# Kernel tuning notes

Measured on AMD Instinct MI355X. Metric: run time of the kernel, lower is better.

The kernel has to match this reference:

```python
import jax, jax.numpy as jnp
import numpy as np


def setup_inputs() -> dict:
    key = jax.random.key(0)
    k1, k2, k3 = jax.random.split(key, 3)
    B, T, C = 4, 2048, 1024
    dim = C
    x = jax.random.normal(k1, (B, T, C), dtype=jnp.float32)
    # torch nn.Linear weight layout: [out_features, in_features], scaled like kaiming-uniform-ish
    w_qkv = jax.random.normal(k2, (3 * dim, dim), dtype=jnp.float32) * (1.0 / np.sqrt(dim))
    w_out = jax.random.normal(k3, (dim, dim), dtype=jnp.float32) * (1.0 / np.sqrt(dim))
    return {"x": x, "w_qkv": w_qkv, "w_out": w_out}


def reference(x, w_qkv, w_out):
    B, T, C = x.shape
    n_heads = 16
    head_dim = C // n_heads

    qkv = jnp.einsum("btc,dc->btd", x, w_qkv)  # [B,T,3C]
    q, k, v = jnp.split(qkv, 3, axis=-1)

    def split_heads(t):
        return t.reshape(B, T, n_heads, head_dim).transpose(0, 2, 1, 3)  # [B,H,T,hd]

    q, k, v = split_heads(q), split_heads(k), split_heads(v)

    scale = 1.0 / np.sqrt(head_dim).astype(np.float32)
    scores = jnp.einsum("bhqd,bhkd->bhqk", q, k) * scale  # [B,H,T,T]
    causal = jnp.tril(jnp.ones((T, T), dtype=bool))
    scores = jnp.where(causal, scores, jnp.finfo(scores.dtype).min)
    attn = jax.nn.softmax(scores, axis=-1)
    out = jnp.einsum("bhqk,bhkd->bhqd", attn, v)  # [B,H,T,hd]
    out = out.transpose(0, 2, 1, 3).reshape(B, T, C)
    return jnp.einsum("btc,dc->btd", out, w_out)
```

## Files before the change

kernel.cpp:

```cpp
#include <hip/hip_runtime.h>
#include <hip/hip_bf16.h>


typedef __attribute__((ext_vector_type(8))) short bf16x8;
typedef __attribute__((ext_vector_type(4))) float f32x4;
typedef __attribute__((ext_vector_type(16))) float f32x16;
typedef __attribute__((ext_vector_type(2))) unsigned uint2v;

#define GLOBAL_AS __attribute__((address_space(1)))
#define LDS_AS __attribute__((address_space(3)))

__device__ __forceinline__ unsigned short f2b_rne(float f) {
  unsigned u = __float_as_uint(f);
  unsigned r = u + 0x7fffu + ((u >> 16) & 1u);
  return (unsigned short)(r >> 16);
}

__device__ __forceinline__ unsigned cvt_pk_bf16(float lo, float hi) {
  unsigned r;
  asm("v_cvt_pk_bf16_f32 %0, %1, %2" : "=v"(r) : "v"(lo), "v"(hi));
  return r;
}

__device__ __forceinline__ void gload_lds16(const void* g, void* l) {
  __builtin_amdgcn_global_load_lds((const GLOBAL_AS void*)g, (LDS_AS void*)l, 16, 0, 0);
}

__global__ void f32_to_bf16_vec(const float* __restrict__ src,
                                unsigned short* __restrict__ dst, int n4) {
  int i = blockIdx.x * blockDim.x + threadIdx.x;
  int stride = gridDim.x * blockDim.x;
  for (; i < n4; i += stride) {
    float4 v = reinterpret_cast<const float4*>(src)[i];
    ushort4 o;
    o.x = f2b_rne(v.x); o.y = f2b_rne(v.y);
    o.z = f2b_rne(v.z); o.w = f2b_rne(v.w);
    reinterpret_cast<ushort4*>(dst)[i] = o;
  }
}

__global__ __launch_bounds__(256)
void v_transpose(const unsigned short* __restrict__ qkv,
                 unsigned short* __restrict__ vt) {
  __shared__ __align__(16) unsigned short Ts[64][64];
  const int tc = blockIdx.x, bh = blockIdx.y;
  const int b = bh >> 4, hed = bh & 15;
  const int t0 = tc * 64;
  const int tid = threadIdx.x;
  {
    const int r = tid >> 2, cb = (tid & 3) * 2;
    const unsigned short* src =
        qkv + (size_t)(b * 2048 + t0 + r) * 3072 + 2048 + hed * 64;
    bf16x8 v0 = *(const bf16x8*)(src + cb * 8);
    bf16x8 v1 = *(const bf16x8*)(src + cb * 8 + 8);
    *(bf16x8*)&Ts[r][(cb ^ (r & 7)) * 8] = v0;
    *(bf16x8*)&Ts[r][((cb + 1) ^ (r & 7)) * 8] = v1;
  }
  __syncthreads();
  const int d = tid >> 2;
  unsigned short* dst = vt + ((size_t)bh * 64 + d) * 2048 + t0;
#pragma unroll
  for (int tb2 = 0; tb2 < 2; ++tb2) {
    int tb = (tid & 3) * 2 + tb2;
    union { unsigned short s[8]; bf16x8 v; } o;
#pragma unroll
    for (int i = 0; i < 8; ++i) {
      int row = tb * 8 + i;
      o.s[i] = Ts[row][(((d >> 3) ^ (row & 7)) * 8) + (d & 7)];
    }
    *(bf16x8*)(dst + tb * 8) = o.v;
  }
}

__global__ __launch_bounds__(512, 2)
void gemm_qkv(const unsigned short* __restrict__ A,
              const unsigned short* __restrict__ B,
              unsigned short* __restrict__ C) {
  const int K = 1024, N = 3072;
  __shared__ __align__(16) unsigned short As[2][2][128 * 64];
  __shared__ __align__(16) unsigned short Bs[2][128 * 64];

  const int tid = threadIdx.x, wid = tid >> 6, lane = tid & 63;
  const int l31 = lane & 31, h = lane >> 5;
  const int wgid = ((int)blockIdx.x & 7) * 96 + ((int)blockIdx.x >> 3);
  const int bx = wgid % 24, by = wgid / 24;
  const int m0 = by * 256, n0 = bx * 128;
  const int wr = wid >> 1, wc = wid & 1;

  auto stage = [&](int t, int buf) {
    const int k0 = t * 64;
    const int r8 = lane >> 3;
    const int blk = (lane & 7) ^ r8;
#pragma unroll
    for (int hh = 0; hh < 2; ++hh)
#pragma unroll
      for (int r = 0; r < 2; ++r) {
        int row = r * 64 + wid * 8 + r8;
        gload_lds16(A + (size_t)(m0 + hh * 128 + row) * K + k0 + blk * 8,
                    &As[buf][hh][r * 4096 + wid * 512]);
      }
#pragma unroll
    for (int r = 0; r < 2; ++r) {
      int row = r * 64 + wid * 8 + r8;
      gload_lds16(B + (size_t)(n0 + row) * K + k0 + blk * 8,
                  &Bs[buf][r * 4096 + wid * 512]);
    }
  };

  f32x16 acc[2][2] = {};

  stage(0, 0);
  asm volatile("s_waitcnt vmcnt(0)" ::: "memory");
  __builtin_amdgcn_sched_barrier(0);
  __builtin_amdgcn_s_barrier();
  __builtin_amdgcn_sched_barrier(0);

  int cur = 0;
  for (int t = 0; t < 16; ++t) {
    if (t + 1 < 16) stage(t + 1, cur ^ 1);

    bf16x8 af[2][4], bfr[2][4];
#pragma unroll
    for (int mi = 0; mi < 2; ++mi) {
      int row = (wr & 1) * 64 + mi * 32 + l31;
#pragma unroll
      for (int ks = 0; ks < 4; ++ks) {
        int chunk = (ks * 2 + h) ^ (row & 7);
        af[mi][ks] = *(const bf16x8*)&As[cur][wr >> 1][row * 64 + chunk * 8];
      }
    }
#pragma unroll
    for (int ni = 0; ni < 2; ++ni) {
      int row = wc * 64 + ni * 32 + l31;
#pragma unroll
      for (int ks = 0; ks < 4; ++ks) {
        int chunk = (ks * 2 + h) ^ (row & 7);
        bfr[ni][ks] = *(const bf16x8*)&Bs[cur][row * 64 + chunk * 8];
      }
    }
    __builtin_amdgcn_s_setprio(1);
#pragma unroll
    for (int ks = 0; ks < 4; ++ks)
#pragma unroll
      for (int mi = 0; mi < 2; ++mi)
#pragma unroll
        for (int ni = 0; ni < 2; ++ni)
          acc[mi][ni] = __builtin_amdgcn_mfma_f32_32x32x16_bf16(
              af[mi][ks], bfr[ni][ks], acc[mi][ni], 0, 0, 0);
    __builtin_amdgcn_s_setprio(0);

    asm volatile("s_waitcnt vmcnt(0)" ::: "memory");
    __builtin_amdgcn_sched_barrier(0);
    __builtin_amdgcn_s_barrier();
    __builtin_amdgcn_sched_barrier(0);
    cur ^= 1;
  }

#pragma unroll
  for (int mi = 0; mi < 2; ++mi)
#pragma unroll
    for (int ni = 0; ni < 2; ++ni)
#pragma unroll
      for (int reg = 0; reg < 16; ++reg) {
        int row = m0 + wr * 64 + mi * 32 + (reg & 3) + 8 * (reg >> 2) + 4 * h;
        int col = n0 + wc * 64 + ni * 32 + l31;
        C[(size_t)row * N + col] = f2b_rne(acc[mi][ni][reg]);
      }
}

__global__ __launch_bounds__(256)
void gemm_nt(const unsigned short* __restrict__ A,
             const unsigned short* __restrict__ B,
             float* __restrict__ Cout, int M, int N, int K) {
  __shared__ __align__(16) unsigned short As[128][32];
  __shared__ __align__(16) unsigned short Bs[128][32];
  const int tid = threadIdx.x;
  const int w = tid >> 6, lane = tid & 63;
  const int l16 = lane & 15, lg = lane >> 4;
  const int wrow = (w >> 1) * 64, wcol = (w & 1) * 64;
  const int m0 = blockIdx.y * 128, n0 = blockIdx.x * 128;

  f32x4 acc[4][4] = {};

  auto stage = [&](int k0) {
#pragma unroll
    for (int c2 = 0; c2 < 2; ++c2) {
      int c = 2 * w + c2;
      const unsigned short* ga =
          A + (size_t)(m0 + 16 * c + (lane >> 2)) * K + k0 + (lane & 3) * 8;
      gload_lds16(ga, &As[16 * c][0]);
      const unsigned short* gb =
          B + (size_t)(n0 + 16 * c + (lane >> 2)) * K + k0 + (lane & 3) * 8;
      gload_lds16(gb, &Bs[16 * c][0]);
    }
  };

  stage(0);
  __syncthreads();
  const int nk = K >> 5;
  for (int ks = 0; ks < nk; ++ks) {
    bf16x8 af[4], bfr[4];
#pragma unroll
    for (int mi = 0; mi < 4; ++mi)
      af[mi] = *(const bf16x8*)&As[wrow + mi * 16 + l16][lg * 8];
#pragma unroll
    for (int ni = 0; ni < 4; ++ni)
      bfr[ni] = *(const bf16x8*)&Bs[wcol + ni * 16 + l16][lg * 8];
    __syncthreads();
    if (ks + 1 < nk) stage((ks + 1) * 32);
#pragma unroll
    for (int mi = 0; mi < 4; ++mi)
#pragma unroll
      for (int ni = 0; ni < 4; ++ni)
        acc[mi][ni] = __builtin_amdgcn_mfma_f32_16x16x32_bf16(
            af[mi], bfr[ni], acc[mi][ni], 0, 0, 0);
    __syncthreads();
  }

#pragma unroll
  for (int mi = 0; mi < 4; ++mi)
#pragma unroll
    for (int ni = 0; ni < 4; ++ni)
#pragma unroll
      for (int j = 0; j < 4; ++j) {
        int row = m0 + wrow + mi * 16 + lg * 4 + j;
        int col = n0 + wcol + ni * 16 + l16;
        Cout[(size_t)row * N + col] = acc[mi][ni][j];
      }
}

__global__ __launch_bounds__(256)
void attn_fwd(const unsigned short* __restrict__ qkv,
              const unsigned short* __restrict__ vt,
              unsigned short* __restrict__ out) {
  const int T = 2048, C3 = 3072;
  __shared__ __align__(16) unsigned short Ks[2][64][64];
  __shared__ __align__(16) unsigned short Vs[2][64][64];
  __shared__ float Bc[4][32];

  const int tid = threadIdx.x, w = tid >> 6, lane = tid & 63;
  const int l31 = lane & 31, h = lane >> 5;
  const int wgid = (blockIdx.x & 7) * 128 + (blockIdx.x >> 3);
  const int qt = 15 - (wgid & 15);
  const int bh = wgid >> 4;
  const int b = bh >> 4, hed = bh & 15;
  const int qw = qt * 128 + w * 32;
  const size_t rowbase = (size_t)b * T * C3;
  const int hoff = hed * 64;
  const unsigned short* vbase = vt + (size_t)bh * 64 * 2048;
  const float c2 = 0.18033688f;

  auto stageK = [&](int kv0, int buf) {
#pragma unroll
    for (int pp = 0; pp < 2; ++pp) {
      int chunk = w * 2 + pp;
      int row = chunk * 8 + (lane >> 3);
      int blk = (lane & 7) ^ (lane >> 3);
      gload_lds16(
          qkv + rowbase + (size_t)(kv0 + row) * C3 + 1024 + hoff + blk * 8,
          &Ks[buf][chunk * 8][0]);
    }
  };
  auto stageV = [&](int kv0, int buf) {
#pragma unroll
    for (int pp = 0; pp < 2; ++pp) {
      int chunk = w * 2 + pp;
      int drow = chunk * 8 + (lane >> 3);
      int blk = (lane & 7) ^ (lane >> 3);
      gload_lds16(vbase + (size_t)drow * 2048 + kv0 + blk * 8,
                  &Vs[buf][chunk * 8][0]);
    }
  };

  bf16x8 qf[4];
  {
    const unsigned short* qp =
        qkv + rowbase + (size_t)(qw + l31) * C3 + hoff + h * 8;
#pragma unroll
    for (int s = 0; s < 4; ++s) qf[s] = *(const bf16x8*)(qp + 16 * s);
  }

  f32x16 oacc[2] = {};
  float m_r = -1e30f, sum = 0.f;

  stageK(0, 0);
  stageV(0, 0);

  int cur = 0;
  const int ntiles = qt * 2 + 2;
  for (int t = 0; t < ntiles; ++t) {
    const int kv0 = t * 64;
    __builtin_amdgcn_s_barrier();
    if (t + 1 < ntiles) {
      stageK(kv0 + 64, cur ^ 1);
      stageV(kv0 + 64, cur ^ 1);
      asm volatile("s_waitcnt vmcnt(4)" ::: "memory");
    } else {
      asm volatile("s_waitcnt vmcnt(0)" ::: "memory");
    }
    __builtin_amdgcn_s_barrier();
    __builtin_amdgcn_sched_barrier(0);

    if (kv0 <= qw) {
      f32x16 sacc[2] = {};
      __builtin_amdgcn_s_setprio(1);
#pragma unroll
      for (int s = 0; s < 4; ++s) {
#pragma unroll
        for (int kt = 0; kt < 2; ++kt) {
          int row = kt * 32 + l31;
          int blk = (2 * s + h) ^ (row & 7);
          bf16x8 kf = *(const bf16x8*)&Ks[cur][row][blk * 8];
          sacc[kt] = __builtin_amdgcn_mfma_f32_32x32x16_bf16(kf, qf[s],
                                                             sacc[kt], 0, 0, 0);
        }
      }
      __builtin_amdgcn_s_setprio(0);
      if (kv0 + 64 > qw) {
        int q_abs = qw + l31;
#pragma unroll
        for (int kt = 0; kt < 2; ++kt)
#pragma unroll
          for (int r = 0; r < 16; ++r) {
            int kv_abs = kv0 + kt * 32 + (r & 3) + 8 * (r >> 2) + 4 * h;
            if (kv_abs > q_abs) sacc[kt][r] = -1e30f;
          }
      }
      float mx[8];
#pragma unroll
      for (int g = 0; g < 8; ++g)
        mx[g] = fmaxf(fmaxf(sacc[g >> 2][(g & 3) * 4 + 0],
                            sacc[g >> 2][(g & 3) * 4 + 1]),
                      fmaxf(sacc[g >> 2][(g & 3) * 4 + 2],
                            sacc[g >> 2][(g & 3) * 4 + 3]));
      float tm = fmaxf(fmaxf(fmaxf(mx[0], mx[1]), fmaxf(mx[2], mx[3])),
                       fmaxf(fmaxf(mx[4], mx[5]), fmaxf(mx[6], mx[7])));
      tm = fmaxf(tm, __shfl_xor(tm, 32));
      if (t == 0) {
        m_r = tm;
      } else if (!__all(tm <= m_r + 16.0f)) {
        float mnew = fmaxf(m_r, tm);
        float corr = __builtin_amdgcn_exp2f((m_r - mnew) * c2);
        sum *= corr;
        if (h == 0) Bc[w][l31] = corr;
        m_r = mnew;
        asm volatile("s_waitcnt lgkmcnt(0)" ::: "memory");
#pragma unroll
        for (int r = 0; r < 16; ++r) {
          float cr = Bc[w][(r & 3) + 8 * (r >> 2) + 4 * h];
          oacc[0][r] *= cr;
          oacc[1][r] *= cr;
        }
      }
      float m2 = m_r * c2;
      float s0 = 0.f, s1 = 0.f, s2 = 0.f, s3 = 0.f;
#pragma unroll
      for (int kt = 0; kt < 2; ++kt)
#pragma unroll
        for (int r = 0; r < 16; r += 4) {
          float p0 = __builtin_amdgcn_exp2f(fmaf(sacc[kt][r + 0], c2, -m2));
          float p1 = __builtin_amdgcn_exp2f(fmaf(sacc[kt][r + 1], c2, -m2));
          float p2 = __builtin_amdgcn_exp2f(fmaf(sacc[kt][r + 2], c2, -m2));
          float p3 = __builtin_amdgcn_exp2f(fmaf(sacc[kt][r + 3], c2, -m2));
          sacc[kt][r + 0] = p0; sacc[kt][r + 1] = p1;
          sacc[kt][r + 2] = p2; sacc[kt][r + 3] = p3;
          s0 += p0; s1 += p1; s2 += p2; s3 += p3;
        }
      float sl = (s0 + s1) + (s2 + s3);
      sum += sl + __shfl_xor(sl, 32);
      unsigned pk[16];
#pragma unroll
      for (int kt = 0; kt < 2; ++kt)
#pragma unroll
        for (int r = 0; r < 16; r += 2)
          pk[kt * 8 + (r >> 1)] = cvt_pk_bf16(sacc[kt][r], sacc[kt][r + 1]);
      __builtin_amdgcn_s_setprio(1);
#pragma unroll
      for (int sg = 0; sg < 4; ++sg) {
        const int kt = sg >> 1, s = sg & 1;
        const int base = kt * 8 + 4 * s;
        uint2v r02 = __builtin_amdgcn_permlane32_swap(pk[base], pk[base + 2],
                                                      false, false);
        uint2v r13 = __builtin_amdgcn_permlane32_swap(pk[base + 1], pk[base + 3],
                                                      false, false);
        union { unsigned u[4]; bf16x8 v; } Afr;
        Afr.u[0] = r02.x; Afr.u[1] = r13.x;
        Afr.u[2] = r02.y; Afr.u[3] = r13.y;
#pragma unroll
        for (int dt = 0; dt < 2; ++dt) {
          int d = dt * 32 + l31;
          int blk = (2 * sg + h) ^ (d & 7);
          bf16x8 vf = *(const bf16x8*)&Vs[cur][d][blk * 8];
          oacc[dt] = __builtin_amdgcn_mfma_f32_32x32x16_bf16(Afr.v, vf,
                                                             oacc[dt], 0, 0, 0);
        }
      }
      __builtin_amdgcn_s_setprio(0);
    }
    cur ^= 1;
  }

  if (h == 0) Bc[w][l31] = 1.0f / sum;
  asm volatile("s_waitcnt lgkmcnt(0)" ::: "memory");
#pragma unroll
  for (int r = 0; r < 16; ++r) {
    int ql = (r & 3) + 8 * (r >> 2) + 4 * h;
    float inv = Bc[w][ql];
    int q_abs = qw + ql;
#pragma unroll
    for (int dt = 0; dt < 2; ++dt) {
      out[(size_t)(b * T + q_abs) * 1024 + hoff + dt * 32 + l31] =
          f2b_rne(oacc[dt][r] * inv);
    }
  }
}

extern "C" void kernel_launch(void* const* d_in, const int* in_sizes, int n_in,
                              void* d_out, int out_size, void* d_ws,
                              size_t ws_size, hipStream_t stream) {
  const float* x = (const float*)d_in[0];
  const float* w_qkv = (const float*)d_in[1];
  const float* w_out = (const float*)d_in[2];
  float* out = (float*)d_out;

  const int M = 8192, C = 1024, C3 = 3072;

  unsigned short* xb = (unsigned short*)d_ws;
  unsigned short* wqkvb = xb + (size_t)M * C;
  unsigned short* woutb = wqkvb + (size_t)C3 * C;
  unsigned short* qkv = woutb + (size_t)C * C;
  unsigned short* vtb = qkv + (size_t)M * C3;
  unsigned short* attno = xb;

  f32_to_bf16_vec<<<1024, 256, 0, stream>>>(x, xb, M * C / 4);
  f32_to_bf16_vec<<<512, 256, 0, stream>>>(w_qkv, wqkvb, C3 * C / 4);
  f32_to_bf16_vec<<<256, 256, 0, stream>>>(w_out, woutb, C * C / 4);

  gemm_qkv<<<768, 512, 0, stream>>>(xb, wqkvb, qkv);

  v_transpose<<<dim3(32, 64), 256, 0, stream>>>(qkv, vtb);

  attn_fwd<<<1024, 256, 0, stream>>>(qkv, vtb, attno);

  gemm_nt<<<dim3(C / 128, M / 128), 256, 0, stream>>>(attno, woutb, out,
                                                      M, C, C);
}
```

Before: 203.5 us.

## Double per-wave query rows in attention to reuse K/V tiles across two halves

```diff
diff --git a/kernel.cpp b/kernel.cpp
--- a/kernel.cpp
+++ b/kernel.cpp
@@ -229,7 +229,7 @@
       }
 }
 
-__global__ __launch_bounds__(256)
+__global__ __launch_bounds__(256, 2)
 void attn_fwd(const unsigned short* __restrict__ qkv,
               const unsigned short* __restrict__ vt,
               unsigned short* __restrict__ out) {
@@ -240,11 +240,13 @@
 
   const int tid = threadIdx.x, w = tid >> 6, lane = tid & 63;
   const int l31 = lane & 31, h = lane >> 5;
-  const int wgid = (blockIdx.x & 7) * 128 + (blockIdx.x >> 3);
-  const int qt = 15 - (wgid & 15);
-  const int bh = wgid >> 4;
+  const int wgid = (blockIdx.x & 7) * 64 + (blockIdx.x >> 3);
+  const int local = wgid & 63, xcd = wgid >> 6;
+  const int qidx = local >> 3, bhl = local & 7;
+  const int bh = xcd * 8 + bhl;
+  const int qt = (qidx < 4) ? (7 - qidx) : (qidx - 4);
   const int b = bh >> 4, hed = bh & 15;
-  const int qw = qt * 128 + w * 32;
+  const int qw = qt * 256 + w * 64;
   const size_t rowbase = (size_t)b * T * C3;
   const int hoff = hed * 64;
   const unsigned short* vbase = vt + (size_t)bh * 64 * 2048;
@@ -272,22 +274,110 @@
     }
   };
 
-  bf16x8 qf[4];
+  bf16x8 qf0[4], qf1[4];
   {
-    const unsigned short* qp =
+    const unsigned short* qp0 =
         qkv + rowbase + (size_t)(qw + l31) * C3 + hoff + h * 8;
-#pragma unroll
-    for (int s = 0; s < 4; ++s) qf[s] = *(const bf16x8*)(qp + 16 * s);
-  }
-
-  f32x16 oacc[2] = {};
-  float m_r = -1e30f, sum = 0.f;
+    const unsigned short* qp1 = qp0 + 32 * C3;
+#pragma unroll
+    for (int s = 0; s < 4; ++s) {
+      qf0[s] = *(const bf16x8*)(qp0 + 16 * s);
+      qf1[s] = *(const bf16x8*)(qp1 + 16 * s);
+    }
+  }
+
+  f32x16 oacc0[2] = {}, oacc1[2] = {};
+  float mr0 = -1e30f, mr1 = -1e30f, sum0 = 0.f, sum1 = 0.f;
 
   stageK(0, 0);
   stageV(0, 0);
 
+  auto do_half = [&](f32x16 (&sacc)[2], int qx, float& mr, float& sm,
+                     f32x16 (&oc)[2], int t, int kv0, int cur) {
+    if (kv0 + 64 > qx) {
+      int q_abs = qx + l31;
+#pragma unroll
+      for (int kt = 0; kt < 2; ++kt)
+#pragma unroll
+        for (int r = 0; r < 16; ++r) {
+          int kv_abs = kv0 + kt * 32 + (r & 3) + 8 * (r >> 2) + 4 * h;
+          if (kv_abs > q_abs) sacc[kt][r] = -1e30f;
+        }
+    }
+    float mx[8];
+#pragma unroll
+    for (int g = 0; g < 8; ++g)
+      mx[g] = fmaxf(fmaxf(sacc[g >> 2][(g & 3) * 4 + 0],
+                          sacc[g >> 2][(g & 3) * 4 + 1]),
+                    fmaxf(sacc[g >> 2][(g & 3) * 4 + 2],
+                          sacc[g >> 2][(g & 3) * 4 + 3]));
+    float tm = fmaxf(fmaxf(fmaxf(mx[0], mx[1]), fmaxf(mx[2], mx[3])),
+                     fmaxf(fmaxf(mx[4], mx[5]), fmaxf(mx[6], mx[7])));
+    tm = fmaxf(tm, __shfl_xor(tm, 32));
+    if (t == 0) {
+      mr = tm;
+    } else if (!__all(tm <= mr + 16.0f)) {
+      float mnew = fmaxf(mr, tm);
+      float corr = __builtin_amdgcn_exp2f((mr - mnew) * c2);
+      sm *= corr;
+      if (h == 0) Bc[w][l31] = corr;
+      mr = mnew;
+      asm volatile("s_waitcnt lgkmcnt(0)" ::: "memory");
+#pragma unroll
+      for (int r = 0; r < 16; ++r) {
+        float cr = Bc[w][(r & 3) + 8 * (r >> 2) + 4 * h];
+        oc[0][r] *= cr;
+        oc[1][r] *= cr;
+      }
+    }
+    float m2 = mr * c2;
+    float s0 = 0.f, s1 = 0.f, s2 = 0.f, s3 = 0.f;
+#pragma unroll
+    for (int kt = 0; kt < 2; ++kt)
+#pragma unroll
+      for (int r = 0; r < 16; r += 4) {
+        float p0 = __builtin_amdgcn_exp2f(fmaf(sacc[kt][r + 0], c2, -m2));
+        float p1 = __builtin_amdgcn_exp2f(fmaf(sacc[kt][r + 1], c2, -m2));
+        float p2 = __builtin_amdgcn_exp2f(fmaf(sacc[kt][r + 2], c2, -m2));
+        float p3 = __builtin_amdgcn_exp2f(fmaf(sacc[kt][r + 3], c2, -m2));
+        sacc[kt][r + 0] = p0; sacc[kt][r + 1] = p1;
+        sacc[kt][r + 2] = p2; sacc[kt][r + 3] = p3;
+        s0 += p0; s1 += p1; s2 += p2; s3 += p3;
+      }
+    float sl = (s0 + s1) + (s2 + s3);
+    sm += sl + __shfl_xor(sl, 32);
+    unsigned pk[16];
+#pragma unroll
+    for (int kt = 0; kt < 2; ++kt)
+#pragma unroll
+      for (int r = 0; r < 16; r += 2)
+        pk[kt * 8 + (r >> 1)] = cvt_pk_bf16(sacc[kt][r], sacc[kt][r + 1]);
+    __builtin_amdgcn_s_setprio(1);
+#pragma unroll
+    for (int sg = 0; sg < 4; ++sg) {
+      const int kt = sg >> 1, s = sg & 1;
+      const int base = kt * 8 + 4 * s;
+      uint2v r02 = __builtin_amdgcn_permlane32_swap(pk[base], pk[base + 2],
+                                                    false, false);
+      uint2v r13 = __builtin_amdgcn_permlane32_swap(pk[base + 1], pk[base + 3],
+                                                    false, false);
+      union { unsigned u[4]; bf16x8 v; } Afr;
+      Afr.u[0] = r02.x; Afr.u[1] = r13.x;
+      Afr.u[2] = r02.y; Afr.u[3] = r13.y;
+#pragma unroll
+      for (int dt = 0; dt < 2; ++dt) {
+        int d = dt * 32 + l31;
+        int blk = (2 * sg + h) ^ (d & 7);
+        bf16x8 vf = *(const bf16x8*)&Vs[cur][d][blk * 8];
+        oc[dt] = __builtin_amdgcn_mfma_f32_32x32x16_bf16(Afr.v, vf,
+                                                         oc[dt], 0, 0, 0);
+      }
+    }
+    __builtin_amdgcn_s_setprio(0);
+  };
+
   int cur = 0;
-  const int ntiles = qt * 2 + 2;
+  const int ntiles = 4 * qt + 4;
   for (int t = 0; t < ntiles; ++t) {
     const int kv0 = t * 64;
     __builtin_amdgcn_s_barrier();
@@ -302,7 +392,7 @@
     __builtin_amdgcn_sched_barrier(0);
 
     if (kv0 <= qw) {
-      f32x16 sacc[2] = {};
+      f32x16 sacc0[2] = {}, sacc1[2] = {};
       __builtin_amdgcn_s_setprio(1);
 #pragma unroll
       for (int s = 0; s < 4; ++s) {
@@ -311,107 +401,37 @@
           int row = kt * 32 + l31;
           int blk = (2 * s + h) ^ (row & 7);
           bf16x8 kf = *(const bf16x8*)&Ks[cur][row][blk * 8];
-          sacc[kt] = __builtin_amdgcn_mfma_f32_32x32x16_bf16(kf, qf[s],
-                                                             sacc[kt], 0, 0, 0);
+          sacc0[kt] = __builtin_amdgcn_mfma_f32_32x32x16_bf16(kf, qf0[s],
+                                                              sacc0[kt], 0, 0, 0);
+          sacc1[kt] = __builtin_amdgcn_mfma_f32_32x32x16_bf16(kf, qf1[s],
+                                                              sacc1[kt], 0, 0, 0);
         }
       }
       __builtin_amdgcn_s_setprio(0);
-      if (kv0 + 64 > qw) {
-        int q_abs = qw + l31;
-#pragma unroll
-        for (int kt = 0; kt < 2; ++kt)
-#pragma unroll
-          for (int r = 0; r < 16; ++r) {
-            int kv_abs = kv0 + kt * 32 + (r & 3) + 8 * (r >> 2) + 4 * h;
-            if (kv_abs > q_abs) sacc[kt][r] = -1e30f;
-          }
-      }
-      float mx[8];
-#pragma unroll
-      for (int g = 0; g < 8; ++g)
-        mx[g] = fmaxf(fmaxf(sacc[g >> 2][(g & 3) * 4 + 0],
-                            sacc[g >> 2][(g & 3) * 4 + 1]),
-                      fmaxf(sacc[g >> 2][(g & 3) * 4 + 2],
-                            sacc[g >> 2][(g & 3) * 4 + 3]));
-      float tm = fmaxf(fmaxf(fmaxf(mx[0], mx[1]), fmaxf(mx[2], mx[3])),
-                       fmaxf(fmaxf(mx[4], mx[5]), fmaxf(mx[6], mx[7])));
-      tm = fmaxf(tm, __shfl_xor(tm, 32));
-      if (t == 0) {
-        m_r = tm;
-      } else if (!__all(tm <= m_r + 16.0f)) {
-        float mnew = fmaxf(m_r, tm);
-        float corr = __builtin_amdgcn_exp2f((m_r - mnew) * c2);
-        sum *= corr;
-        if (h == 0) Bc[w][l31] = corr;
-        m_r = mnew;
-        asm volatile("s_waitcnt lgkmcnt(0)" ::: "memory");
-#pragma unroll
-        for (int r = 0; r < 16; ++r) {
-          float cr = Bc[w][(r & 3) + 8 * (r >> 2) + 4 * h];
-          oacc[0][r] *= cr;
-          oacc[1][r] *= cr;
-        }
-      }
-      float m2 = m_r * c2;
-      float s0 = 0.f, s1 = 0.f, s2 = 0.f, s3 = 0.f;
-#pragma unroll
-      for (int kt = 0; kt < 2; ++kt)
-#pragma unroll
-        for (int r = 0; r < 16; r += 4) {
-          float p0 = __builtin_amdgcn_exp2f(fmaf(sacc[kt][r + 0], c2, -m2));
-          float p1 = __builtin_amdgcn_exp2f(fmaf(sacc[kt][r + 1], c2, -m2));
-          float p2 = __builtin_amdgcn_exp2f(fmaf(sacc[kt][r + 2], c2, -m2));
-          float p3 = __builtin_amdgcn_exp2f(fmaf(sacc[kt][r + 3], c2, -m2));
-          sacc[kt][r + 0] = p0; sacc[kt][r + 1] = p1;
-          sacc[kt][r + 2] = p2; sacc[kt][r + 3] = p3;
-          s0 += p0; s1 += p1; s2 += p2; s3 += p3;
-        }
-      float sl = (s0 + s1) + (s2 + s3);
-      sum += sl + __shfl_xor(sl, 32);
-      unsigned pk[16];
-#pragma unroll
-      for (int kt = 0; kt < 2; ++kt)
-#pragma unroll
-        for (int r = 0; r < 16; r += 2)
-          pk[kt * 8 + (r >> 1)] = cvt_pk_bf16(sacc[kt][r], sacc[kt][r + 1]);
-      __builtin_amdgcn_s_setprio(1);
-#pragma unroll
-      for (int sg = 0; sg < 4; ++sg) {
-        const int kt = sg >> 1, s = sg & 1;
-        const int base = kt * 8 + 4 * s;
-        uint2v r02 = __builtin_amdgcn_permlane32_swap(pk[base], pk[base + 2],
-                                                      false, false);
-        uint2v r13 = __builtin_amdgcn_permlane32_swap(pk[base + 1], pk[base + 3],
-                                                      false, false);
-        union { unsigned u[4]; bf16x8 v; } Afr;
-        Afr.u[0] = r02.x; Afr.u[1] = r13.x;
-        Afr.u[2] = r02.y; Afr.u[3] = r13.y;
-#pragma unroll
-        for (int dt = 0; dt < 2; ++dt) {
-          int d = dt * 32 + l31;
-          int blk = (2 * sg + h) ^ (d & 7);
-          bf16x8 vf = *(const bf16x8*)&Vs[cur][d][blk * 8];
-          oacc[dt] = __builtin_amdgcn_mfma_f32_32x32x16_bf16(Afr.v, vf,
-                                                             oacc[dt], 0, 0, 0);
-        }
-      }
-      __builtin_amdgcn_s_setprio(0);
+      do_half(sacc0, qw, mr0, sum0, oacc0, t, kv0, cur);
+      do_half(sacc1, qw + 32, mr1, sum1, oacc1, t, kv0, cur);
     }
     cur ^= 1;
   }
 
-  if (h == 0) Bc[w][l31] = 1.0f / sum;
-  asm volatile("s_waitcnt lgkmcnt(0)" ::: "memory");
-#pragma unroll
-  for (int r = 0; r < 16; ++r) {
-    int ql = (r & 3) + 8 * (r >> 2) + 4 * h;
-    float inv = Bc[w][ql];
-    int q_abs = qw + ql;
-#pragma unroll
-    for (int dt = 0; dt < 2; ++dt) {
-      out[(size_t)(b * T + q_abs) * 1024 + hoff + dt * 32 + l31] =
-          f2b_rne(oacc[dt][r] * inv);
-    }
+#pragma unroll
+  for (int X = 0; X < 2; ++X) {
+    float sm = X ? sum1 : sum0;
+    if (h == 0) Bc[w][l31] = 1.0f / sm;
+    asm volatile("s_waitcnt lgkmcnt(0)" ::: "memory");
+#pragma unroll
+    for (int r = 0; r < 16; ++r) {
+      int ql = (r & 3) + 8 * (r >> 2) + 4 * h;
+      float inv = Bc[w][ql];
+      int q_abs = qw + 32 * X + ql;
+#pragma unroll
+      for (int dt = 0; dt < 2; ++dt) {
+        float v = (X ? oacc1 : oacc0)[dt][r] * inv;
+        out[(size_t)(b * T + q_abs) * 1024 + hoff + dt * 32 + l31] =
+            f2b_rne(v);
+      }
+    }
+    __builtin_amdgcn_s_barrier();
   }
 }
 
@@ -440,7 +460,7 @@
 
   v_transpose<<<dim3(32, 64), 256, 0, stream>>>(qkv, vtb);
 
-  attn_fwd<<<1024, 256, 0, stream>>>(qkv, vtb, attno);
+  attn_fwd<<<512, 256, 0, stream>>>(qkv, vtb, attno);
 
   gemm_nt<<<dim3(C / 128, M / 128), 256, 0, stream>>>(attno, woutb, out,
                                                       M, C, C);
```

Result: faster. 192.2 us (-5.6%).
